# Kernel optimization log

Measured on AMD Instinct MI355X. Metric: run time of the kernel, lower is better.

The kernel has to match this reference:

```python
import jax, jax.numpy as jnp
import numpy as np

B, N, D, H = 4, 2048, 512, 8
DK = D // H
NEG_SLOPE = 0.1


def setup_inputs() -> dict:
    key = jax.random.key(0)
    k_x, k_m, k_qkv, k_o, k_b = jax.random.split(key, 5)
    x = jax.random.normal(k_x, (B, N, D), dtype=jnp.float32)
    mask = jax.random.randint(k_m, (B, N, N), 0, 2).astype(bool)
    # guarantee self-edges so no row is fully masked (avoids NaN softmax)
    mask = mask | jnp.eye(N, dtype=bool)[None]
    scale = 1.0 / np.sqrt(D)
    Wqkv = jax.random.normal(k_qkv, (D, 3 * D), dtype=jnp.float32) * scale
    Wout = jax.random.normal(k_o, (D, D), dtype=jnp.float32) * scale
    bout = jax.random.normal(k_b, (D,), dtype=jnp.float32) * 0.01
    return {"x": x, "mask": mask, "Wqkv": Wqkv, "Wout": Wout, "bout": bout}


def reference(x, mask, Wqkv, Wout, bout):
    # x: (B,N,D), mask: (B,N,N) bool (True = keep edge)
    qkv = x @ Wqkv                               # (B,N,3D)
    q, k, v = jnp.split(qkv, 3, axis=-1)

    def heads(t):
        return t.reshape(B, N, H, DK).transpose(0, 2, 1, 3)  # (B,H,N,DK)

    q, k, v = heads(q), heads(k), heads(v)
    scores = jnp.einsum('bhnd,bhmd->bhnm', q, k) / np.sqrt(DK)  # (B,H,N,N)
    scores = jnp.where(mask[:, None], scores, -jnp.inf)
    attn = jax.nn.softmax(scores, axis=-1)
    out = jnp.einsum('bhnm,bhmd->bhnd', attn, v)               # (B,H,N,DK)
    out = out.transpose(0, 2, 1, 3).reshape(B, N, D)
    out = out @ Wout + bout
    return jnp.where(out >= 0, out, NEG_SLOPE * out)            # LeakyReLU
```

## Files before the change

### kernel.cpp

```cpp
#include <hip/hip_runtime.h>
#include <stdint.h>

#define Bb 4
#define Nn 2048
#define Dd 512
#define Hh 8
#define BN 8192

typedef __attribute__((ext_vector_type(4))) float f32x4;
typedef __attribute__((ext_vector_type(8))) short s16x8;

#define QSCALE 0.1803368801111204f

static constexpr size_t OFF_XB    = 1024;
static constexpr size_t OFF_WQKVT = OFF_XB    + (size_t)2 * BN * Dd;
static constexpr size_t OFF_WOUTT = OFF_WQKVT + (size_t)2 * 3 * Dd * Dd;
static constexpr size_t OFF_MASKP = OFF_WOUTT + (size_t)2 * Dd * Dd;
static constexpr size_t OFF_Q     = OFF_MASKP + (size_t)8 * Bb * Nn * (Nn / 64);
static constexpr size_t OFF_K     = OFF_Q     + (size_t)2 * BN * Dd;
static constexpr size_t OFF_VT    = OFF_K     + (size_t)2 * BN * Dd;
static constexpr size_t OFF_AO    = OFF_VT    + (size_t)2 * BN * Dd;

__device__ inline unsigned short f2bf(float f) {
  union { float f; unsigned int u; } v; v.f = f;
  const unsigned int u = v.u;
  return (unsigned short)((u + 0x7fffu + ((u >> 16) & 1u)) >> 16);
}

__device__ inline float exp2_hw(float x) {
  float r;
  asm("v_exp_f32 %0, %1" : "=v"(r) : "v"(x));
  return r;
}

__device__ inline unsigned int cvtpk_bf16(float lo, float hi) {
  unsigned int r;
  asm("v_cvt_pk_bf16_f32 %0, %1, %2" : "=v"(r) : "v"(lo), "v"(hi));
  return r;
}

__device__ inline void gload16(const void* g, void* l) {
  __builtin_amdgcn_global_load_lds(
      (const __attribute__((address_space(1))) uint32_t*)g,
      (__attribute__((address_space(3))) uint32_t*)l, 16, 0, 0);
}

__global__ void prep_kernel(const float* __restrict__ x, unsigned short* __restrict__ xb,
                            const float* __restrict__ Wqkv, unsigned short* __restrict__ wqkvT,
                            const float* __restrict__ Wout, unsigned short* __restrict__ woutT,
                            const unsigned char* __restrict__ mb, const int* __restrict__ mi,
                            unsigned long long* __restrict__ mp) {
  __shared__ float tsm[64][65];
  const int bid = blockIdx.x, tid = threadIdx.x;
  if (bid < 2048) {
    for (int i = bid * 256 + tid; i < BN * Dd / 4; i += 2048 * 256) {
      const float4 v = ((const float4*)x)[i];
      ushort4 o;
      o.x = f2bf(v.x); o.y = f2bf(v.y); o.z = f2bf(v.z); o.w = f2bf(v.w);
      ((ushort4*)xb)[i] = o;
    }
  } else if (bid < 2304) {
    const float* W; unsigned short* WT; int C, tt;
    if (bid < 2240) { W = Wqkv; WT = wqkvT; C = 1536; tt = bid - 2048; }
    else            { W = Wout; WT = woutT; C = 512;  tt = bid - 2240; }
    const int tcols = C >> 6;
    const int rt = tt / tcols, ct = tt - rt * tcols;
    const int r0 = rt * 64, c0t = ct * 64;
    {
      const int row = tid >> 4, colq = tid & 15;
#pragma unroll
      for (int rr = 0; rr < 4; ++rr) {
        const float4 v = *(const float4*)&W[(size_t)(r0 + rr * 16 + row) * C + c0t + colq * 4];
        tsm[rr * 16 + row][colq * 4 + 0] = v.x;
        tsm[rr * 16 + row][colq * 4 + 1] = v.y;
        tsm[rr * 16 + row][colq * 4 + 2] = v.z;
        tsm[rr * 16 + row][colq * 4 + 3] = v.w;
      }
    }
    __syncthreads();
    {
      const int ocl = tid >> 2, seg = tid & 3;
      unsigned short ob[16];
#pragma unroll
      for (int j = 0; j < 16; ++j) ob[j] = f2bf(tsm[seg * 16 + j][ocl]);
      unsigned short* dst = WT + (size_t)(c0t + ocl) * 512 + r0 + seg * 16;
      *(s16x8*)dst = *(s16x8*)ob;
      *(s16x8*)(dst + 8) = *(s16x8*)(ob + 8);
    }
  } else {
    const int lane = tid & 63;
    const int ok = mb[(size_t)(lane + 1) * (Nn + 1)] != 0;
    const int bytemode = (__ballot(ok) == 0xFFFFFFFFFFFFFFFFull);
    const int nwords = Bb * Nn * (Nn / 64);
    int gw = ((bid - 2304) * 256 + tid) >> 6;
    for (; gw < nwords; gw += 1024 * 4) {
      const size_t idx = (size_t)gw * 64 + lane;
      int v;
      if (bytemode) v = mb[idx]; else v = mi[idx];
      const unsigned long long bits = __ballot(v != 0);
      if (lane == 0) mp[gw] = bits;
    }
  }
}

template <int MODE, int BNt>
__global__ __launch_bounds__(256, 2) void gemm128(
    const unsigned short* __restrict__ A,
    const unsigned short* __restrict__ BT,
    unsigned short* __restrict__ qb, unsigned short* __restrict__ kb,
    unsigned short* __restrict__ vt, const float* __restrict__ bias,
    float* __restrict__ outp) {
  constexpr int JN = BNt / 32;
  constexpr int BBYTES = BNt * 128;
  __shared__ char smem[32768 + 2 * BBYTES];
  const int tid = threadIdx.x;
  const int lane = tid & 63, wv = tid >> 6;
  const int g = lane >> 4, n16 = lane & 15;
  const int bid = blockIdx.x;
  const int xcd = bid & 7, tt = bid >> 3;
  const int gx = xcd * 8 + (tt & 7);
  const int gy = tt >> 3;
  const int m0 = gx * 128;
  const int c0 = gy * BNt;
  const int wm = wv >> 1, wn = wv & 1;

  f32x4 acc[4][JN] = {};

  auto stage = [&](int buf, int t) {
#pragma unroll
    for (int j = 0; j < 4; ++j) {
      const int base = (wv * 4 + j) * 1024;
      const int o = base + lane * 16;
      const int r = o >> 7;
      const int sl = ((o >> 4) & 7) ^ (r & 7);
      gload16(A + (size_t)(m0 + r) * 512 + t * 64 + sl * 8, smem + buf * 16384 + base);
    }
#pragma unroll
    for (int j = 0; j < BNt / 32; ++j) {
      const int base = (wv * (BNt / 32) + j) * 1024;
      const int o = base + lane * 16;
      const int r = o >> 7;
      const int sl = ((o >> 4) & 7) ^ (r & 7);
      gload16(BT + (size_t)(c0 + r) * 512 + t * 64 + sl * 8, smem + 32768 + buf * BBYTES + base);
    }
  };

  stage(0, 0);
  __syncthreads();
  int cur = 0;
  for (int t = 0; t < 8; ++t) {
    if (t < 7) stage(cur ^ 1, t + 1);
    const unsigned short* Ab = (const unsigned short*)(smem + cur * 16384);
    const unsigned short* Bbuf = (const unsigned short*)(smem + 32768 + cur * BBYTES);
    s16x8 af[4][2], bfr[JN][2];
#pragma unroll
    for (int f = 0; f < 4; ++f)
#pragma unroll
      for (int kc = 0; kc < 2; ++kc) {
        const int rr = wm * 64 + f * 16 + n16;
        const int sl = kc * 4 + g;
        af[f][kc] = *(const s16x8*)&Ab[(rr * 128 + ((sl ^ (rr & 7)) * 16)) / 2];
      }
#pragma unroll
    for (int f = 0; f < JN; ++f)
#pragma unroll
      for (int kc = 0; kc < 2; ++kc) {
        const int cc = wn * (BNt / 2) + f * 16 + n16;
        const int sl = kc * 4 + g;
        bfr[f][kc] = *(const s16x8*)&Bbuf[(cc * 128 + ((sl ^ (cc & 7)) * 16)) / 2];
      }
    __builtin_amdgcn_s_setprio(1);
#pragma unroll
    for (int i = 0; i < 4; ++i)
#pragma unroll
      for (int jn = 0; jn < JN; ++jn) {
        acc[i][jn] = __builtin_amdgcn_mfma_f32_16x16x32_bf16(af[i][0], bfr[jn][0], acc[i][jn], 0, 0, 0);
        acc[i][jn] = __builtin_amdgcn_mfma_f32_16x16x32_bf16(af[i][1], bfr[jn][1], acc[i][jn], 0, 0, 0);
      }
    __builtin_amdgcn_s_setprio(0);
    __syncthreads();
    cur ^= 1;
  }

  if (MODE == 0) {
    const int bq = m0 >> 11, nn0 = m0 & 2047;
    if (c0 < 1024) {
#pragma unroll
      for (int i = 0; i < 4; ++i) {
        const int tl0 = wm * 64 + i * 16 + g * 4;
#pragma unroll
        for (int jn = 0; jn < JN; ++jn) {
          const int c = c0 + wn * 64 + jn * 16 + n16;
          if (c < 512) {
            const int h = c >> 6, dk = c & 63;
            unsigned short* qp = qb + (((size_t)bq * 8 + h) * 2048 + nn0 + tl0) * 64 + dk;
#pragma unroll
            for (int r = 0; r < 4; ++r) qp[(size_t)r * 64] = f2bf(acc[i][jn][r] * QSCALE);
          } else {
            const int c2 = c - 512, h = c2 >> 6, dk = c2 & 63;
            unsigned short* kp = kb + (((size_t)bq * 8 + h) * 2048 + nn0 + tl0) * 64 + dk;
#pragma unroll
            for (int r = 0; r < 4; ++r) kp[(size_t)r * 64] = f2bf(acc[i][jn][r]);
          }
        }
      }
    } else {
      constexpr int SW = 136;
      unsigned short* Ep = (unsigned short*)smem;
#pragma unroll
      for (int i = 0; i < 4; ++i) {
        const int tl0 = wm * 64 + i * 16 + g * 4;
#pragma unroll
        for (int jn = 0; jn < JN; ++jn) {
          const int cl = wn * 64 + jn * 16 + n16;
          ushort4 pk;
          pk.x = f2bf(acc[i][jn][0]); pk.y = f2bf(acc[i][jn][1]);
          pk.z = f2bf(acc[i][jn][2]); pk.w = f2bf(acc[i][jn][3]);
          *(ushort4*)&Ep[cl * SW + (tl0 ^ (((cl >> 3) & 7) << 3))] = pk;
        }
      }
      __syncthreads();
#pragma unroll
      for (int itc = 0; itc < 8; ++itc) {
        const int chunk = itc * 256 + tid;
        const int cl = chunk >> 4, tc = chunk & 15;
        const s16x8 v = *(const s16x8*)&Ep[cl * SW + ((tc * 8) ^ (((cl >> 3) & 7) << 3))];
        const int c2 = c0 + cl - 1024;
        const int h = c2 >> 6, dk = c2 & 63;
        *(s16x8*)(vt + (((size_t)bq * 8 + h) * 64 + dk) * 2048 + nn0 + tc * 8) = v;
      }
    }
  } else {
#pragma unroll
    for (int jn = 0; jn < JN; ++jn) {
      const int c = c0 + wn * (BNt / 2) + jn * 16 + n16;
      const float bc = bias[c];
#pragma unroll
      for (int i = 0; i < 4; ++i) {
        const int tok0 = m0 + wm * 64 + i * 16 + g * 4;
#pragma unroll
        for (int r = 0; r < 4; ++r) {
          float v = acc[i][jn][r] + bc;
          v = v >= 0.f ? v : 0.1f * v;
          outp[(size_t)(tok0 + r) * 512 + c] = v;
        }
      }
    }
  }
}

__global__ __launch_bounds__(512, 6) void attn_kernel(
    const unsigned short* __restrict__ qb, const unsigned short* __restrict__ kb,
    const unsigned short* __restrict__ vt, const unsigned long long* __restrict__ mp,
    unsigned short* __restrict__ ao) {
  __shared__ unsigned short Kl[2][4096];
  __shared__ unsigned short Vl[2][4096];
  __shared__ unsigned short Pl[8][1024];
  const int tid = threadIdx.x, lane = tid & 63, wv = tid >> 6;
  const int g = lane >> 4, n16 = lane & 15;
  const int sbid = (blockIdx.x & 7) * 64 + (blockIdx.x >> 3);
  const int qt = sbid & 15, bh = sbid >> 4;
  const int b = bh >> 3, h = bh & 7;
  const int n0 = qt * 128 + wv * 16;
  const unsigned short* Qh = qb + (size_t)bh * 2048 * 64;
  const unsigned short* Kh = kb + (size_t)bh * 2048 * 64;
  const unsigned short* Vh = vt + (size_t)bh * 64 * 2048;
  const unsigned long long* mrow = mp + ((size_t)b * 2048 + n0 + n16) * 32;

  const s16x8 qf0 = *(const s16x8*)&Qh[(size_t)(n0 + n16) * 64 + g * 8];
  const s16x8 qf1 = *(const s16x8*)&Qh[(size_t)(n0 + n16) * 64 + 32 + g * 8];

  const s16x8 ones = {0x3F80, 0x3F80, 0x3F80, 0x3F80, 0x3F80, 0x3F80, 0x3F80, 0x3F80};

  f32x4 of[4] = {};
  f32x4 acc_l = {};

  unsigned short* Pw = Pl[wv];
  int pwo[4], pro[2];
#pragma unroll
  for (int mf = 0; mf < 4; ++mf) {
    int bo = n16 * 128 + mf * 32 + g * 8;
    pwo[mf] = bo ^ ((n16 & 7) << 4);
  }
#pragma unroll
  for (int kc = 0; kc < 2; ++kc) {
    int bo = n16 * 128 + kc * 64 + g * 16;
    pro[kc] = bo ^ ((n16 & 7) << 4);
  }

  auto stage = [&](int buf, int m0) {
    const int base = wv * 1024;
    const int o = base + lane * 16;
    const int r = o >> 7;
    const int sl = ((o >> 4) & 7) ^ (r & 7);
    gload16(Kh + (size_t)(m0 + r) * 64 + sl * 8, (char*)&Kl[buf][0] + base);
    gload16(Vh + (size_t)r * 2048 + m0 + sl * 8, (char*)&Vl[buf][0] + base);
  };

  stage(0, 0);
  unsigned long long wbits = mrow[0];
  __syncthreads();
  int cur = 0;
  for (int it = 0; it < 32; ++it) {
    if (it < 31) stage(cur ^ 1, (it + 1) * 64);
    const unsigned long long wnext = (it < 31) ? mrow[it + 1] : 0ull;

    f32x4 sc[4] = {};
    __builtin_amdgcn_s_setprio(1);
#pragma unroll
    for (int mf = 0; mf < 4; ++mf) {
      const int ml = mf * 16 + n16;
#pragma unroll
      for (int kc = 0; kc < 2; ++kc) {
        const int sl = kc * 4 + g;
        const s16x8 kf = *(const s16x8*)&Kl[cur][(ml * 128 + ((sl ^ (ml & 7)) * 16)) / 2];
        sc[mf] = __builtin_amdgcn_mfma_f32_16x16x32_bf16(kf, kc ? qf1 : qf0, sc[mf], 0, 0, 0);
      }
    }
    __builtin_amdgcn_s_setprio(0);

    const unsigned int wlo = (unsigned int)(wbits >> (g * 4));
    const unsigned int whi = (unsigned int)(wbits >> (32 + g * 4));

    unsigned int w[8];
#pragma unroll
    for (int mf = 0; mf < 4; ++mf) {
      const unsigned int wsel = ((mf & 2) ? whi : wlo) >> ((mf & 1) * 16);
      float p[4];
#pragma unroll
      for (int r = 0; r < 4; ++r) {
        const unsigned int sm = (unsigned int)__builtin_amdgcn_sbfe((int)wsel, r, 1);
        const float pv = exp2_hw(sc[mf][r]);
        p[r] = __uint_as_float(__float_as_uint(pv) & sm);
      }
      w[mf * 2]     = cvtpk_bf16(p[0], p[1]);
      w[mf * 2 + 1] = cvtpk_bf16(p[2], p[3]);
    }

#pragma unroll
    for (int mf = 0; mf < 4; ++mf) {
      uint2 pk2; pk2.x = w[mf * 2]; pk2.y = w[mf * 2 + 1];
      *(uint2*)((char*)Pw + pwo[mf]) = pk2;
    }
    __builtin_amdgcn_s_setprio(1);
#pragma unroll
    for (int kc = 0; kc < 2; ++kc) {
      const s16x8 pf = *(const s16x8*)((const char*)Pw + pro[kc]);
      acc_l = __builtin_amdgcn_mfma_f32_16x16x32_bf16(pf, ones, acc_l, 0, 0, 0);
#pragma unroll
      for (int df = 0; df < 4; ++df) {
        const int dk = df * 16 + n16;
        const int sl = kc * 4 + g;
        const s16x8 vf = *(const s16x8*)&Vl[cur][(dk * 128 + ((sl ^ (dk & 7)) * 16)) / 2];
        of[df] = __builtin_amdgcn_mfma_f32_16x16x32_bf16(pf, vf, of[df], 0, 0, 0);
      }
    }
    __builtin_amdgcn_s_setprio(0);
    wbits = wnext;
    __syncthreads();
    cur ^= 1;
  }

  float rinv[4];
#pragma unroll
  for (int r = 0; r < 4; ++r) rinv[r] = 1.f / acc_l[r];
#pragma unroll
  for (int df = 0; df < 4; ++df)
#pragma unroll
    for (int r = 0; r < 4; ++r) {
      const int token = b * 2048 + n0 + 4 * g + r;
      ao[(size_t)token * 512 + h * 64 + df * 16 + n16] = f2bf(of[df][r] * rinv[r]);
    }
}

extern "C" void kernel_launch(void* const* d_in, const int* in_sizes, int n_in,
                              void* d_out, int out_size, void* d_ws, size_t ws_size,
                              hipStream_t stream) {
  const float* x = (const float*)d_in[0];
  const void* mask = d_in[1];
  const float* Wqkv = (const float*)d_in[2];
  const float* Wout = (const float*)d_in[3];
  const float* bout = (const float*)d_in[4];
  float* out = (float*)d_out;
  char* ws = (char*)d_ws;

  unsigned short* xb = (unsigned short*)(ws + OFF_XB);
  unsigned short* wqkvT = (unsigned short*)(ws + OFF_WQKVT);
  unsigned short* woutT = (unsigned short*)(ws + OFF_WOUTT);
  unsigned long long* mp = (unsigned long long*)(ws + OFF_MASKP);
  unsigned short* qb = (unsigned short*)(ws + OFF_Q);
  unsigned short* kb = (unsigned short*)(ws + OFF_K);
  unsigned short* vt = (unsigned short*)(ws + OFF_VT);
  unsigned short* ao = (unsigned short*)(ws + OFF_AO);

  prep_kernel<<<3328, 256, 0, stream>>>(x, xb, Wqkv, wqkvT, Wout, woutT,
                                        (const unsigned char*)mask, (const int*)mask, mp);
  gemm128<0, 128><<<768, 256, 0, stream>>>(xb, wqkvT, qb, kb, vt, nullptr, nullptr);
  attn_kernel<<<512, 512, 0, stream>>>(qb, kb, vt, mp, ao);
  gemm128<1, 64><<<512, 256, 0, stream>>>(ao, woutT, nullptr, nullptr, nullptr, bout, out);
}
```

Baseline: 120.4 us.

## Transpose packed mask layout and stage mask words through LDS with explicit vmcnt waits

The packed-mask producer now writes words in a (batch, key-tile, query-row) layout, so one 64-key tile of mask bits for a 128-row query block is contiguous. The attention kernel loads these bits with the same async global-to-LDS loads it uses for K/V tiles, double-buffered, instead of each lane doing a scalar global read per iteration. The __syncthreads calls become raw s_barrier plus explicit s_waitcnt vmcnt counts and sched_barriers, so the next tile's loads can stay in flight across the barrier. The cost is an extra LDS buffer, and correctness now depends on the hand-counted vmcnt values.

```diff
diff --git a/kernel.cpp b/kernel.cpp
--- a/kernel.cpp
+++ b/kernel.cpp
@@ -11,6 +11,8 @@
 typedef __attribute__((ext_vector_type(8))) short s16x8;
 
 #define QSCALE 0.1803368801111204f
+
+#define VMCNT(n) asm volatile("s_waitcnt vmcnt(" #n ")" ::: "memory")
 
 static constexpr size_t OFF_XB    = 1024;
 static constexpr size_t OFF_WQKVT = OFF_XB    + (size_t)2 * BN * Dd;
@@ -94,7 +96,10 @@
     const int nwords = Bb * Nn * (Nn / 64);
     int gw = ((bid - 2304) * 256 + tid) >> 6;
     for (; gw < nwords; gw += 1024 * 4) {
-      const size_t idx = (size_t)gw * 64 + lane;
+      const int row = gw & 2047;
+      const int t = (gw >> 11) & 31;
+      const int bb = gw >> 16;
+      const size_t idx = ((size_t)bb * 2048 + row) * 2048 + t * 64 + lane;
       int v;
       if (bytemode) v = mb[idx]; else v = mi[idx];
       const unsigned long long bits = __ballot(v != 0);
@@ -256,6 +261,7 @@
   __shared__ unsigned short Kl[2][4096];
   __shared__ unsigned short Vl[2][4096];
   __shared__ unsigned short Pl[8][1024];
+  __shared__ unsigned long long Ml[2][128];
   const int tid = threadIdx.x, lane = tid & 63, wv = tid >> 6;
   const int g = lane >> 4, n16 = lane & 15;
   const int sbid = (blockIdx.x & 7) * 64 + (blockIdx.x >> 3);
@@ -265,7 +271,7 @@
   const unsigned short* Qh = qb + (size_t)bh * 2048 * 64;
   const unsigned short* Kh = kb + (size_t)bh * 2048 * 64;
   const unsigned short* Vh = vt + (size_t)bh * 64 * 2048;
-  const unsigned long long* mrow = mp + ((size_t)b * 2048 + n0 + n16) * 32;
+  const unsigned long long* Mh = mp + (size_t)b * 32 * 2048 + qt * 128;
 
   const s16x8 qf0 = *(const s16x8*)&Qh[(size_t)(n0 + n16) * 64 + g * 8];
   const s16x8 qf1 = *(const s16x8*)&Qh[(size_t)(n0 + n16) * 64 + 32 + g * 8];
@@ -288,22 +294,33 @@
     pro[kc] = bo ^ ((n16 & 7) << 4);
   }
 
-  auto stage = [&](int buf, int m0) {
+  const int lr = wv * 16 + n16;
+
+  auto stage = [&](int buf, int t) {
     const int base = wv * 1024;
     const int o = base + lane * 16;
     const int r = o >> 7;
     const int sl = ((o >> 4) & 7) ^ (r & 7);
-    gload16(Kh + (size_t)(m0 + r) * 64 + sl * 8, (char*)&Kl[buf][0] + base);
-    gload16(Vh + (size_t)r * 2048 + m0 + sl * 8, (char*)&Vl[buf][0] + base);
+    gload16(Kh + (size_t)(t * 64 + r) * 64 + sl * 8, (char*)&Kl[buf][0] + base);
+    gload16(Vh + (size_t)r * 2048 + t * 64 + sl * 8, (char*)&Vl[buf][0] + base);
+    gload16(Mh + (size_t)t * 2048 + lane * 2, (char*)&Ml[buf][0]);
   };
 
   stage(0, 0);
-  unsigned long long wbits = mrow[0];
-  __syncthreads();
+  VMCNT(0);
+  __builtin_amdgcn_s_barrier();
   int cur = 0;
   for (int it = 0; it < 32; ++it) {
-    if (it < 31) stage(cur ^ 1, (it + 1) * 64);
-    const unsigned long long wnext = (it < 31) ? mrow[it + 1] : 0ull;
+    if (it < 31) {
+      stage(cur ^ 1, it + 1);
+      VMCNT(3);
+    } else {
+      VMCNT(0);
+    }
+    __builtin_amdgcn_s_barrier();
+    __builtin_amdgcn_sched_barrier(0);
+
+    const unsigned long long wbits = Ml[cur][lr];
 
     f32x4 sc[4] = {};
     __builtin_amdgcn_s_setprio(1);
@@ -356,8 +373,8 @@
       }
     }
     __builtin_amdgcn_s_setprio(0);
-    wbits = wnext;
-    __syncthreads();
+    __builtin_amdgcn_sched_barrier(0);
+    __builtin_amdgcn_s_barrier();
     cur ^= 1;
   }
 
```

After: 122.1 us. Within noise of the previous version (+1.4%).

## Process two query tiles per wave in attention to reuse K/V fragments

Applied to the files above, without the earlier changes.

The attention block drops from 8 waves to 4, and each wave now handles two 16-row query tiles instead of one. Each K and V fragment read from LDS feeds two MFMAs, which halves LDS read traffic per unit of compute and gives the scheduler more independent MFMA chains to interleave. In exchange each wave holds more accumulator and query registers, and each block has fewer waves to hide latency, so occupancy can drop.

```diff
diff --git a/kernel.cpp b/kernel.cpp
--- a/kernel.cpp
+++ b/kernel.cpp
@@ -249,7 +249,7 @@
   }
 }
 
-__global__ __launch_bounds__(512, 6) void attn_kernel(
+__global__ __launch_bounds__(256, 3) void attn_kernel(
     const unsigned short* __restrict__ qb, const unsigned short* __restrict__ kb,
     const unsigned short* __restrict__ vt, const unsigned long long* __restrict__ mp,
     unsigned short* __restrict__ ao) {
@@ -261,21 +261,26 @@
   const int sbid = (blockIdx.x & 7) * 64 + (blockIdx.x >> 3);
   const int qt = sbid & 15, bh = sbid >> 4;
   const int b = bh >> 3, h = bh & 7;
-  const int n0 = qt * 128 + wv * 16;
+  const int n0A = qt * 128 + wv * 16;
+  const int n0B = n0A + 64;
   const unsigned short* Qh = qb + (size_t)bh * 2048 * 64;
   const unsigned short* Kh = kb + (size_t)bh * 2048 * 64;
   const unsigned short* Vh = vt + (size_t)bh * 64 * 2048;
-  const unsigned long long* mrow = mp + ((size_t)b * 2048 + n0 + n16) * 32;
-
-  const s16x8 qf0 = *(const s16x8*)&Qh[(size_t)(n0 + n16) * 64 + g * 8];
-  const s16x8 qf1 = *(const s16x8*)&Qh[(size_t)(n0 + n16) * 64 + 32 + g * 8];
+  const unsigned long long* mrowA = mp + ((size_t)b * 2048 + n0A + n16) * 32;
+  const unsigned long long* mrowB = mp + ((size_t)b * 2048 + n0B + n16) * 32;
+
+  const s16x8 qfA0 = *(const s16x8*)&Qh[(size_t)(n0A + n16) * 64 + g * 8];
+  const s16x8 qfA1 = *(const s16x8*)&Qh[(size_t)(n0A + n16) * 64 + 32 + g * 8];
+  const s16x8 qfB0 = *(const s16x8*)&Qh[(size_t)(n0B + n16) * 64 + g * 8];
+  const s16x8 qfB1 = *(const s16x8*)&Qh[(size_t)(n0B + n16) * 64 + 32 + g * 8];
 
   const s16x8 ones = {0x3F80, 0x3F80, 0x3F80, 0x3F80, 0x3F80, 0x3F80, 0x3F80, 0x3F80};
 
-  f32x4 of[4] = {};
-  f32x4 acc_l = {};
-
-  unsigned short* Pw = Pl[wv];
+  f32x4 ofA[4] = {}, ofB[4] = {};
+  f32x4 accA = {}, accB = {};
+
+  unsigned short* PwA = Pl[wv * 2];
+  unsigned short* PwB = Pl[wv * 2 + 1];
   int pwo[4], pro[2];
 #pragma unroll
   for (int mf = 0; mf < 4; ++mf) {
@@ -289,23 +294,45 @@
   }
 
   auto stage = [&](int buf, int m0) {
-    const int base = wv * 1024;
-    const int o = base + lane * 16;
-    const int r = o >> 7;
-    const int sl = ((o >> 4) & 7) ^ (r & 7);
-    gload16(Kh + (size_t)(m0 + r) * 64 + sl * 8, (char*)&Kl[buf][0] + base);
-    gload16(Vh + (size_t)r * 2048 + m0 + sl * 8, (char*)&Vl[buf][0] + base);
+#pragma unroll
+    for (int j = 0; j < 2; ++j) {
+      const int base = (wv * 2 + j) * 1024;
+      const int o = base + lane * 16;
+      const int r = o >> 7;
+      const int sl = ((o >> 4) & 7) ^ (r & 7);
+      gload16(Kh + (size_t)(m0 + r) * 64 + sl * 8, (char*)&Kl[buf][0] + base);
+      gload16(Vh + (size_t)r * 2048 + m0 + sl * 8, (char*)&Vl[buf][0] + base);
+    }
   };
 
+  auto packP = [&](unsigned long long wb, const f32x4* sc, unsigned int* w) {
+    const unsigned int wlo = (unsigned int)(wb >> (g * 4));
+    const unsigned int whi = (unsigned int)(wb >> (32 + g * 4));
+#pragma unroll
+    for (int mf = 0; mf < 4; ++mf) {
+      const unsigned int wsel = ((mf & 2) ? whi : wlo) >> ((mf & 1) * 16);
+      float p[4];
+#pragma unroll
+      for (int r = 0; r < 4; ++r) {
+        const unsigned int sm = (unsigned int)__builtin_amdgcn_sbfe((int)wsel, r, 1);
+        const float pv = exp2_hw(sc[mf][r]);
+        p[r] = __uint_as_float(__float_as_uint(pv) & sm);
+      }
+      w[mf * 2]     = cvtpk_bf16(p[0], p[1]);
+      w[mf * 2 + 1] = cvtpk_bf16(p[2], p[3]);
+    }
+  };
+
   stage(0, 0);
-  unsigned long long wbits = mrow[0];
+  unsigned long long wbitsA = mrowA[0], wbitsB = mrowB[0];
   __syncthreads();
   int cur = 0;
   for (int it = 0; it < 32; ++it) {
     if (it < 31) stage(cur ^ 1, (it + 1) * 64);
-    const unsigned long long wnext = (it < 31) ? mrow[it + 1] : 0ull;
-
-    f32x4 sc[4] = {};
+    const unsigned long long wnextA = (it < 31) ? mrowA[it + 1] : 0ull;
+    const unsigned long long wnextB = (it < 31) ? mrowB[it + 1] : 0ull;
+
+    f32x4 scA[4] = {}, scB[4] = {};
     __builtin_amdgcn_s_setprio(1);
 #pragma unroll
     for (int mf = 0; mf < 4; ++mf) {
@@ -314,62 +341,56 @@
       for (int kc = 0; kc < 2; ++kc) {
         const int sl = kc * 4 + g;
         const s16x8 kf = *(const s16x8*)&Kl[cur][(ml * 128 + ((sl ^ (ml & 7)) * 16)) / 2];
-        sc[mf] = __builtin_amdgcn_mfma_f32_16x16x32_bf16(kf, kc ? qf1 : qf0, sc[mf], 0, 0, 0);
+        scA[mf] = __builtin_amdgcn_mfma_f32_16x16x32_bf16(kf, kc ? qfA1 : qfA0, scA[mf], 0, 0, 0);
+        scB[mf] = __builtin_amdgcn_mfma_f32_16x16x32_bf16(kf, kc ? qfB1 : qfB0, scB[mf], 0, 0, 0);
       }
     }
     __builtin_amdgcn_s_setprio(0);
 
-    const unsigned int wlo = (unsigned int)(wbits >> (g * 4));
-    const unsigned int whi = (unsigned int)(wbits >> (32 + g * 4));
-
-    unsigned int w[8];
+    unsigned int wA[8], wB[8];
+    packP(wbitsA, scA, wA);
+    packP(wbitsB, scB, wB);
+
 #pragma unroll
     for (int mf = 0; mf < 4; ++mf) {
-      const unsigned int wsel = ((mf & 2) ? whi : wlo) >> ((mf & 1) * 16);
-      float p[4];
-#pragma unroll
-      for (int r = 0; r < 4; ++r) {
-        const unsigned int sm = (unsigned int)__builtin_amdgcn_sbfe((int)wsel, r, 1);
-        const float pv = exp2_hw(sc[mf][r]);
-        p[r] = __uint_as_float(__float_as_uint(pv) & sm);
-      }
-      w[mf * 2]     = cvtpk_bf16(p[0], p[1]);
-      w[mf * 2 + 1] = cvtpk_bf16(p[2], p[3]);
-    }
-
-#pragma unroll
-    for (int mf = 0; mf < 4; ++mf) {
-      uint2 pk2; pk2.x = w[mf * 2]; pk2.y = w[mf * 2 + 1];
-      *(uint2*)((char*)Pw + pwo[mf]) = pk2;
+      uint2 pkA; pkA.x = wA[mf * 2]; pkA.y = wA[mf * 2 + 1];
+      *(uint2*)((char*)PwA + pwo[mf]) = pkA;
+      uint2 pkB; pkB.x = wB[mf * 2]; pkB.y = wB[mf * 2 + 1];
+      *(uint2*)((char*)PwB + pwo[mf]) = pkB;
     }
     __builtin_amdgcn_s_setprio(1);
 #pragma unroll
     for (int kc = 0; kc < 2; ++kc) {
-      const s16x8 pf = *(const s16x8*)((const char*)Pw + pro[kc]);
-      acc_l = __builtin_amdgcn_mfma_f32_16x16x32_bf16(pf, ones, acc_l, 0, 0, 0);
+      const s16x8 pfA = *(const s16x8*)((const char*)PwA + pro[kc]);
+      const s16x8 pfB = *(const s16x8*)((const char*)PwB + pro[kc]);
+      accA = __builtin_amdgcn_mfma_f32_16x16x32_bf16(pfA, ones, accA, 0, 0, 0);
+      accB = __builtin_amdgcn_mfma_f32_16x16x32_bf16(pfB, ones, accB, 0, 0, 0);
 #pragma unroll
       for (int df = 0; df < 4; ++df) {
         const int dk = df * 16 + n16;
         const int sl = kc * 4 + g;
         const s16x8 vf = *(const s16x8*)&Vl[cur][(dk * 128 + ((sl ^ (dk & 7)) * 16)) / 2];
-        of[df] = __builtin_amdgcn_mfma_f32_16x16x32_bf16(pf, vf, of[df], 0, 0, 0);
+        ofA[df] = __builtin_amdgcn_mfma_f32_16x16x32_bf16(pfA, vf, ofA[df], 0, 0, 0);
+        ofB[df] = __builtin_amdgcn_mfma_f32_16x16x32_bf16(pfB, vf, ofB[df], 0, 0, 0);
       }
     }
     __builtin_amdgcn_s_setprio(0);
-    wbits = wnext;
+    wbitsA = wnextA; wbitsB = wnextB;
     __syncthreads();
     cur ^= 1;
   }
 
-  float rinv[4];
-#pragma unroll
-  for (int r = 0; r < 4; ++r) rinv[r] = 1.f / acc_l[r];
+  float rinvA[4], rinvB[4];
+#pragma unroll
+  for (int r = 0; r < 4; ++r) { rinvA[r] = 1.f / accA[r]; rinvB[r] = 1.f / accB[r]; }
 #pragma unroll
   for (int df = 0; df < 4; ++df)
 #pragma unroll
     for (int r = 0; r < 4; ++r) {
-      const int token = b * 2048 + n0 + 4 * g + r;
-      ao[(size_t)token * 512 + h * 64 + df * 16 + n16] = f2bf(of[df][r] * rinv[r]);
+      const int tokA = b * 2048 + n0A + 4 * g + r;
+      ao[(size_t)tokA * 512 + h * 64 + df * 16 + n16] = f2bf(ofA[df][r] * rinvA[r]);
+      const int tokB = b * 2048 + n0B + 4 * g + r;
+      ao[(size_t)tokB * 512 + h * 64 + df * 16 + n16] = f2bf(ofB[df][r] * rinvB[r]);
     }
 }
 
@@ -396,6 +417,6 @@
   prep_kernel<<<3328, 256, 0, stream>>>(x, xb, Wqkv, wqkvT, Wout, woutT,
                                         (const unsigned char*)mask, (const int*)mask, mp);
   gemm128<0, 128><<<768, 256, 0, stream>>>(xb, wqkvT, qb, kb, vt, nullptr, nullptr);
-  attn_kernel<<<512, 512, 0, stream>>>(qb, kb, vt, mp, ao);
+  attn_kernel<<<512, 256, 0, stream>>>(qb, kb, vt, mp, ao);
   gemm128<1, 64><<<512, 256, 0, stream>>>(ao, woutT, nullptr, nullptr, nullptr, bout, out);
 }
```

After: 123.0 us. 2.2% more time.
